# Performance work log

Hardware: AMD Instinct MI355X
Metric: run time of the kernel (lower is better)

## Reference

```python
import jax, jax.numpy as jnp
import numpy as np

B, D_IN, D_HID, E, K = 524288, 256, 512, 16, 2


def setup_inputs() -> dict:
    key = jax.random.key(0)
    kx, k1, kb1, k2, kb2 = jax.random.split(key, 5)
    s1 = 1.0 / np.sqrt(D_IN)
    s2 = 1.0 / np.sqrt(D_HID)
    return {
        "x": jax.random.normal(kx, (B, D_IN), dtype=jnp.float32),
        "w1": jax.random.uniform(k1, (D_IN, D_HID), jnp.float32, -s1, s1),
        "b1": jax.random.uniform(kb1, (D_HID,), jnp.float32, -s1, s1),
        "w2": jax.random.uniform(k2, (D_HID, E), jnp.float32, -s2, s2),
        "b2": jax.random.uniform(kb2, (E,), jnp.float32, -s2, s2),
    }


def reference(x, w1, b1, w2, b2):
    # 2-layer MLP router
    h = jax.nn.relu(x @ w1 + b1)            # [B, D_HID]
    logits = h @ w2 + b2                    # [B, E]
    # top-k mask (1.0 at top-k expert slots, 0.0 elsewhere)
    _, topk_idx = jax.lax.top_k(logits, K)  # [B, K]
    mask = jax.nn.one_hot(topk_idx, E, dtype=logits.dtype).sum(axis=-2)  # [B, E]
    # NOTE: faithful to original — non-topk logits are zeroed (not -inf),
    # then softmax is taken over ALL experts including the zeros.
    sparse_logits = logits * mask
    weights = jax.nn.softmax(sparse_logits, axis=-1)
    return weights
```

## Files before the change

### kernel.cpp

```cpp
#include <hip/hip_runtime.h>
#include <cmath>

#define NE   16
#define DIN  256
#define DHID 512
#define NROW 524288
#define TAU  4e-4f

typedef __bf16 bf16;
typedef bf16  bf16x8 __attribute__((ext_vector_type(8)));
typedef float f32x4  __attribute__((ext_vector_type(4)));

template<int CTRL>
__device__ __forceinline__ float dpp_xor_add(float v) {
    int s = __builtin_amdgcn_update_dpp(0, __float_as_int(v), CTRL, 0xF, 0xF, true);
    return v + __int_as_float(s);
}
template<int OFF>
__device__ __forceinline__ float swz_xor_add(float v) {
    int s = __builtin_amdgcn_ds_swizzle(__float_as_int(v), OFF);
    return v + __int_as_float(s);
}

__global__ __launch_bounds__(256)
void split_w1_k(const float* __restrict__ w1, bf16* __restrict__ t_hi,
                bf16* __restrict__ t_lo) {
    int i = blockIdx.x * 256 + threadIdx.x;
    int col = i & 511, k = i >> 9;
    float v = w1[k * DHID + col];
    bf16 h = (bf16)v;
    t_hi[col * DIN + k] = h;
    t_lo[col * DIN + k] = (bf16)(v - (float)h);
}

__global__ __launch_bounds__(256, 2)
void router_mfma_k(const float* __restrict__ x,
                   const float* __restrict__ b1,
                   const float* __restrict__ w2,
                   const float* __restrict__ b2,
                   float* __restrict__ out,
                   const bf16* __restrict__ w1t_hi,
                   const bf16* __restrict__ w1t_lo,
                   unsigned* __restrict__ cnt,
                   unsigned* __restrict__ ids,
                   unsigned cap)
{
    __shared__ __align__(16) bf16 xh_s[4][129][8];
    __shared__ __align__(16) bf16 xl_s[4][129][8];
    __shared__ __align__(16) bf16 wh_s[4][129][8];
    __shared__ __align__(16) bf16 wl_s[4][129][8];
    __shared__ float l_lds[128][NE + 1];

    const int t    = threadIdx.x;
    const int lane = t & 63;
    const int wv   = t >> 6;
    const int c    = lane & 15;
    const int g    = lane >> 4;
    const long long row0 = (long long)blockIdx.x * 128;

    float lg[8];
#pragma unroll
    for (int i = 0; i < 8; ++i) lg[i] = 0.f;

    for (int ch = 0; ch < 4; ++ch) {
        const int nh0 = ch * 128;
        f32x4 acc[2][8];
#pragma unroll
        for (int ti = 0; ti < 2; ++ti)
#pragma unroll
            for (int tj = 0; tj < 8; ++tj)
#pragma unroll
                for (int r = 0; r < 4; ++r) acc[ti][tj][r] = 0.f;

        for (int ks = 0; ks < 8; ++ks) {
            const int k0 = ks * 32;
            __syncthreads();
#pragma unroll
            for (int u = 0; u < 4; ++u) {
                int idx = u * 256 + t;
                int row = idx >> 3, f4 = idx & 7;
                float4 v = *(const float4*)(x + (row0 + row) * DIN + k0 + f4 * 4);
                int gg = f4 >> 1, j0 = (f4 & 1) * 4;
                bf16* dh = &xh_s[gg][row][j0];
                bf16* dl = &xl_s[gg][row][j0];
                float vv[4] = {v.x, v.y, v.z, v.w};
#pragma unroll
                for (int q = 0; q < 4; ++q) {
                    bf16 hb = (bf16)vv[q];
                    dh[q] = hb;
                    dl[q] = (bf16)(vv[q] - (float)hb);
                }
            }
            {
                int col = t >> 1, half = t & 1;
                const bf16* sh = w1t_hi + (nh0 + col) * DIN + k0 + 16 * half;
                const bf16* sl = w1t_lo + (nh0 + col) * DIN + k0 + 16 * half;
#pragma unroll
                for (int u = 0; u < 2; ++u) {
                    *(bf16x8*)&wh_s[2 * half + u][col][0] = *(const bf16x8*)(sh + 8 * u);
                    *(bf16x8*)&wl_s[2 * half + u][col][0] = *(const bf16x8*)(sl + 8 * u);
                }
            }
            __syncthreads();
            bf16x8 ah[2], al[2];
#pragma unroll
            for (int ti = 0; ti < 2; ++ti) {
                ah[ti] = *(const bf16x8*)&xh_s[g][32 * wv + 16 * ti + c][0];
                al[ti] = *(const bf16x8*)&xl_s[g][32 * wv + 16 * ti + c][0];
            }
#pragma unroll
            for (int tj = 0; tj < 8; ++tj) {
                bf16x8 bh = *(const bf16x8*)&wh_s[g][16 * tj + c][0];
                bf16x8 bl = *(const bf16x8*)&wl_s[g][16 * tj + c][0];
#pragma unroll
                for (int ti = 0; ti < 2; ++ti) {
                    acc[ti][tj] = __builtin_amdgcn_mfma_f32_16x16x32_bf16(ah[ti], bh, acc[ti][tj], 0, 0, 0);
                    acc[ti][tj] = __builtin_amdgcn_mfma_f32_16x16x32_bf16(ah[ti], bl, acc[ti][tj], 0, 0, 0);
                    acc[ti][tj] = __builtin_amdgcn_mfma_f32_16x16x32_bf16(al[ti], bh, acc[ti][tj], 0, 0, 0);
                }
            }
        }

#pragma unroll
        for (int tj = 0; tj < 8; ++tj) {
            float bj = b1[nh0 + 16 * tj + c];
#pragma unroll
            for (int ti = 0; ti < 2; ++ti)
#pragma unroll
                for (int r = 0; r < 4; ++r)
                    acc[ti][tj][r] = fmaxf(acc[ti][tj][r] + bj, 0.f);
        }

#pragma unroll 1
        for (int e = 0; e < NE; ++e) {
            float p[8];
#pragma unroll
            for (int i = 0; i < 8; ++i) p[i] = 0.f;
#pragma unroll
            for (int tj = 0; tj < 8; ++tj) {
                float wvv = w2[(nh0 + 16 * tj + c) * NE + e];
#pragma unroll
                for (int ti = 0; ti < 2; ++ti)
#pragma unroll
                    for (int r = 0; r < 4; ++r)
                        p[ti * 4 + r] = fmaf(acc[ti][tj][r], wvv, p[ti * 4 + r]);
            }
#pragma unroll
            for (int i = 0; i < 8; ++i) p[i] = dpp_xor_add<0xB1>(p[i]);
#pragma unroll
            for (int i = 0; i < 8; ++i) p[i] = dpp_xor_add<0x4E>(p[i]);
#pragma unroll
            for (int i = 0; i < 8; ++i) p[i] = swz_xor_add<0x101F>(p[i]);
#pragma unroll
            for (int i = 0; i < 8; ++i) p[i] = swz_xor_add<0x201F>(p[i]);
            if (c == e) {
#pragma unroll
                for (int i = 0; i < 8; ++i) lg[i] += p[i];
            }
        }
    }

    __syncthreads();
    {
        float b2c = b2[c];
#pragma unroll
        for (int ti = 0; ti < 2; ++ti)
#pragma unroll
            for (int r = 0; r < 4; ++r)
                l_lds[32 * wv + 16 * ti + 4 * g + r][c] = lg[ti * 4 + r] + b2c;
    }
    __syncthreads();

    if (t < 128) {
        float l[NE];
#pragma unroll
        for (int e = 0; e < NE; ++e) l[e] = l_lds[t][e];

        float m1 = -INFINITY; int i1 = 0;
#pragma unroll
        for (int e = 0; e < NE; ++e)
            if (l[e] > m1) { m1 = l[e]; i1 = e; }
        float m2 = -INFINITY; int i2 = -1;
#pragma unroll
        for (int e = 0; e < NE; ++e)
            if (e != i1 && l[e] > m2) { m2 = l[e]; i2 = e; }
        float m3 = -INFINITY;
#pragma unroll
        for (int e = 0; e < NE; ++e)
            if (e != i1 && e != i2 && l[e] > m3) m3 = l[e];

        if (m2 - m3 < TAU) {
            unsigned idx = atomicAdd(cnt, 1u);
            if (idx < cap) ids[idx] = (unsigned)(row0 + t);
        }

        float s[NE];
#pragma unroll
        for (int e = 0; e < NE; ++e)
            s[e] = (e == i1 || e == i2) ? l[e] : 0.f;
        float mx = s[0];
#pragma unroll
        for (int e = 1; e < NE; ++e) mx = fmaxf(mx, s[e]);
        float ex[NE];
        float sum = 0.f;
#pragma unroll
        for (int e = 0; e < NE; ++e) { ex[e] = expf(s[e] - mx); sum += ex[e]; }
        float* og = out + (row0 + t) * NE;
#pragma unroll
        for (int e = 0; e < NE; ++e) og[e] = ex[e] / sum;
    }
}

__global__ __launch_bounds__(256)
void fixup_k(const float* __restrict__ x,
             const float* __restrict__ w1,
             const float* __restrict__ b1,
             const float* __restrict__ w2,
             const float* __restrict__ b2,
             float* __restrict__ out,
             const unsigned* __restrict__ cntp,
             const unsigned* __restrict__ ids,
             unsigned cap)
{
    const int lane = threadIdx.x & 63;
    const int gw   = (int)((blockIdx.x * 256 + threadIdx.x) >> 6);
    const int nw   = (int)((gridDim.x * 256) >> 6);
    unsigned n = *cntp; if (n > cap) n = cap;
    const int c = lane & 15;
    const int g = lane >> 4;

    for (unsigned wi = gw; wi < n; wi += nw) {
        unsigned row = ids[wi];
        const float* xr = x + (size_t)row * DIN;
        const int nh0 = 128 * g;
        int cols[8];
#pragma unroll
        for (int j = 0; j < 8; ++j)
            cols[j] = nh0 + c * 4 + (j & 3) + ((j >> 2) << 6);

        float a[8];
#pragma unroll
        for (int j = 0; j < 8; ++j) a[j] = 0.f;
        for (int k4 = 0; k4 < 64; ++k4) {
            float4 xv = *(const float4*)(xr + k4 * 4);
            const float* wp = w1 + (size_t)(k4 * 4) * DHID;
#pragma unroll
            for (int j = 0; j < 8; ++j) {
                a[j] = fmaf(xv.x, wp[cols[j]],            a[j]);
                a[j] = fmaf(xv.y, wp[DHID + cols[j]],     a[j]);
                a[j] = fmaf(xv.z, wp[2 * DHID + cols[j]], a[j]);
                a[j] = fmaf(xv.w, wp[3 * DHID + cols[j]], a[j]);
            }
        }
        float h[8];
#pragma unroll
        for (int j = 0; j < 8; ++j) h[j] = fmaxf(a[j] + b1[cols[j]], 0.f);

        float l[NE];
#pragma unroll 1
        for (int e = 0; e < NE; ++e) {
            float p = 0.f;
#pragma unroll
            for (int j = 0; j < 8; ++j)
                p = fmaf(h[j], w2[cols[j] * NE + e], p);
            p += __shfl_xor(p, 1, 64);
            p += __shfl_xor(p, 2, 64);
            p += __shfl_xor(p, 4, 64);
            p += __shfl_xor(p, 8, 64);
            float t0 = __shfl(p, 0 * 16 + e, 64);
            float t1 = __shfl(p, 1 * 16 + e, 64);
            float t2 = __shfl(p, 2 * 16 + e, 64);
            float t3 = __shfl(p, 3 * 16 + e, 64);
            l[e] = (((t0 + t1) + t2) + t3) + b2[e];
        }

        if (lane == 0) {
            float m1 = -INFINITY; int i1 = 0;
#pragma unroll
            for (int e = 0; e < NE; ++e)
                if (l[e] > m1) { m1 = l[e]; i1 = e; }
            float m2 = -INFINITY; int i2 = -1;
#pragma unroll
            for (int e = 0; e < NE; ++e)
                if (e != i1 && l[e] > m2) { m2 = l[e]; i2 = e; }
            float s[NE];
#pragma unroll
            for (int e = 0; e < NE; ++e)
                s[e] = (e == i1 || e == i2) ? l[e] : 0.f;
            float mx = s[0];
#pragma unroll
            for (int e = 1; e < NE; ++e) mx = fmaxf(mx, s[e]);
            float ex[NE];
            float sum = 0.f;
#pragma unroll
            for (int e = 0; e < NE; ++e) { ex[e] = expf(s[e] - mx); sum += ex[e]; }
            float* og = out + (size_t)row * NE;
#pragma unroll
            for (int e = 0; e < NE; ++e) og[e] = ex[e] / sum;
        }
    }
}

extern "C" void kernel_launch(void* const* d_in, const int* in_sizes, int n_in,
                              void* d_out, int out_size, void* d_ws, size_t ws_size,
                              hipStream_t stream) {
    const float* x  = (const float*)d_in[0];
    const float* w1 = (const float*)d_in[1];
    const float* b1 = (const float*)d_in[2];
    const float* w2 = (const float*)d_in[3];
    const float* b2 = (const float*)d_in[4];
    float* outp = (float*)d_out;

    bf16*     w1t_hi = (bf16*)d_ws;
    bf16*     w1t_lo = (bf16*)((char*)d_ws + (256u << 10));
    unsigned* cnt    = (unsigned*)((char*)d_ws + (1u << 20));
    unsigned* ids    = (unsigned*)((char*)d_ws + (1u << 20) + 64);
    unsigned  cap    = 0;
    if (ws_size > (1u << 20) + 64)
        cap = (unsigned)((ws_size - (1u << 20) - 64) / 4);

    hipMemsetAsync((char*)d_ws + (1u << 20), 0, 4, stream);
    split_w1_k<<<dim3(512), dim3(256), 0, stream>>>(w1, w1t_hi, w1t_lo);
    router_mfma_k<<<dim3(NROW / 128), dim3(256), 0, stream>>>(
        x, b1, w2, b2, outp, w1t_hi, w1t_lo, cnt, ids, cap);
    fixup_k<<<dim3(256), dim3(256), 0, stream>>>(
        x, w1, b1, w2, b2, outp, cnt, ids, cap);
}
```

Baseline: 1.347 ms.

## Stage x once per block and stream pre-tiled W1 via direct LDS loads

Each block now handles 64 rows and converts its whole x tile to bf16 hi/lo once into shared memory, instead of re-reading and re-splitting x for every hidden chunk. W1 is pre-arranged into the exact LDS tile layout so it can be copied with global_load_lds, and waves are split 2x2 over rows and hidden columns, with partial logits summed through LDS. Output rows are written with vector stores. This cuts repeated global traffic on x at the cost of much larger shared memory per block and more W1 reloads per row.

```diff
diff --git a/kernel.cpp b/kernel.cpp
--- a/kernel.cpp
+++ b/kernel.cpp
@@ -5,6 +5,7 @@
 #define DIN  256
 #define DHID 512
 #define NROW 524288
+#define ROWS 64
 #define TAU  4e-4f
 
 typedef __bf16 bf16;
@@ -21,16 +22,24 @@
     int s = __builtin_amdgcn_ds_swizzle(__float_as_int(v), OFF);
     return v + __int_as_float(s);
 }
+__device__ __forceinline__ void load_lds16(const void* g, void* l) {
+    __builtin_amdgcn_global_load_lds(
+        (const __attribute__((address_space(1))) void*)g,
+        (__attribute__((address_space(3))) void*)l,
+        16, 0, 0);
+}
 
 __global__ __launch_bounds__(256)
-void split_w1_k(const float* __restrict__ w1, bf16* __restrict__ t_hi,
-                bf16* __restrict__ t_lo) {
+void split_w1_k(const float* __restrict__ w1, bf16* __restrict__ w1t) {
     int i = blockIdx.x * 256 + threadIdx.x;
     int col = i & 511, k = i >> 9;
     float v = w1[k * DHID + col];
     bf16 h = (bf16)v;
-    t_hi[col * DIN + k] = h;
-    t_lo[col * DIN + k] = (bf16)(v - (float)h);
+    bf16 l = (bf16)(v - (float)h);
+    int ch = col >> 7, cl = col & 127, ksk = k >> 5, g = (k >> 3) & 3, j = k & 7;
+    size_t base = (size_t)(ch * 8 + ksk) * 8192;
+    w1t[base +        g * 1024 + cl * 8 + j] = h;
+    w1t[base + 4096 + g * 1024 + cl * 8 + j] = l;
 }
 
 __global__ __launch_bounds__(256, 2)
@@ -39,79 +48,81 @@
                    const float* __restrict__ w2,
                    const float* __restrict__ b2,
                    float* __restrict__ out,
-                   const bf16* __restrict__ w1t_hi,
-                   const bf16* __restrict__ w1t_lo,
+                   const bf16* __restrict__ w1t,
                    unsigned* __restrict__ cnt,
                    unsigned* __restrict__ ids,
                    unsigned cap)
 {
-    __shared__ __align__(16) bf16 xh_s[4][129][8];
-    __shared__ __align__(16) bf16 xl_s[4][129][8];
-    __shared__ __align__(16) bf16 wh_s[4][129][8];
-    __shared__ __align__(16) bf16 wl_s[4][129][8];
-    __shared__ float l_lds[128][NE + 1];
+    __shared__ __align__(16) bf16 xh_s[8][4][ROWS][8];
+    __shared__ __align__(16) bf16 xl_s[8][4][ROWS][8];
+    __shared__ __align__(16) bf16 w_s[2][4][128][8];
+    float* l_lds = (float*)&w_s[0][0][0][0];
 
     const int t    = threadIdx.x;
     const int lane = t & 63;
     const int wv   = t >> 6;
+    const int wr   = wv >> 1;
+    const int wc   = wv & 1;
     const int c    = lane & 15;
     const int g    = lane >> 4;
-    const long long row0 = (long long)blockIdx.x * 128;
+    const long long row0 = (long long)blockIdx.x * ROWS;
+
+    {
+        const int r = t & 63;
+        const float* xg = x + (row0 + r) * DIN + wv * 64;
+#pragma unroll
+        for (int m = 0; m < 8; ++m) {
+            float4 v0 = ((const float4*)xg)[2 * m];
+            float4 v1 = ((const float4*)xg)[2 * m + 1];
+            int k   = wv * 64 + m * 8;
+            int ksk = k >> 5, gg = (k >> 3) & 3;
+            float vv[8] = {v0.x, v0.y, v0.z, v0.w, v1.x, v1.y, v1.z, v1.w};
+            bf16 hb[8], lb[8];
+#pragma unroll
+            for (int q = 0; q < 8; ++q) {
+                hb[q] = (bf16)vv[q];
+                lb[q] = (bf16)(vv[q] - (float)hb[q]);
+            }
+            *(bf16x8*)&xh_s[ksk][gg][r][0] = *(const bf16x8*)hb;
+            *(bf16x8*)&xl_s[ksk][gg][r][0] = *(const bf16x8*)lb;
+        }
+    }
 
     float lg[8];
 #pragma unroll
     for (int i = 0; i < 8; ++i) lg[i] = 0.f;
 
     for (int ch = 0; ch < 4; ++ch) {
-        const int nh0 = ch * 128;
-        f32x4 acc[2][8];
+        f32x4 acc[2][4];
 #pragma unroll
         for (int ti = 0; ti < 2; ++ti)
 #pragma unroll
-            for (int tj = 0; tj < 8; ++tj)
+            for (int tj = 0; tj < 4; ++tj)
 #pragma unroll
                 for (int r = 0; r < 4; ++r) acc[ti][tj][r] = 0.f;
 
-        for (int ks = 0; ks < 8; ++ks) {
-            const int k0 = ks * 32;
+        for (int ksk = 0; ksk < 8; ++ksk) {
             __syncthreads();
-#pragma unroll
-            for (int u = 0; u < 4; ++u) {
-                int idx = u * 256 + t;
-                int row = idx >> 3, f4 = idx & 7;
-                float4 v = *(const float4*)(x + (row0 + row) * DIN + k0 + f4 * 4);
-                int gg = f4 >> 1, j0 = (f4 & 1) * 4;
-                bf16* dh = &xh_s[gg][row][j0];
-                bf16* dl = &xl_s[gg][row][j0];
-                float vv[4] = {v.x, v.y, v.z, v.w};
-#pragma unroll
-                for (int q = 0; q < 4; ++q) {
-                    bf16 hb = (bf16)vv[q];
-                    dh[q] = hb;
-                    dl[q] = (bf16)(vv[q] - (float)hb);
-                }
-            }
             {
-                int col = t >> 1, half = t & 1;
-                const bf16* sh = w1t_hi + (nh0 + col) * DIN + k0 + 16 * half;
-                const bf16* sl = w1t_lo + (nh0 + col) * DIN + k0 + 16 * half;
-#pragma unroll
-                for (int u = 0; u < 2; ++u) {
-                    *(bf16x8*)&wh_s[2 * half + u][col][0] = *(const bf16x8*)(sh + 8 * u);
-                    *(bf16x8*)&wl_s[2 * half + u][col][0] = *(const bf16x8*)(sl + 8 * u);
-                }
+                const bf16* src = w1t + (size_t)(ch * 8 + ksk) * 8192
+                                      + wv * 2048 + lane * 8;
+                bf16* dst = ((bf16*)w_s) + wv * 2048;
+#pragma unroll
+                for (int p = 0; p < 4; ++p)
+                    load_lds16(src + p * 512, dst + p * 512);
             }
             __syncthreads();
+
             bf16x8 ah[2], al[2];
 #pragma unroll
             for (int ti = 0; ti < 2; ++ti) {
-                ah[ti] = *(const bf16x8*)&xh_s[g][32 * wv + 16 * ti + c][0];
-                al[ti] = *(const bf16x8*)&xl_s[g][32 * wv + 16 * ti + c][0];
-            }
-#pragma unroll
-            for (int tj = 0; tj < 8; ++tj) {
-                bf16x8 bh = *(const bf16x8*)&wh_s[g][16 * tj + c][0];
-                bf16x8 bl = *(const bf16x8*)&wl_s[g][16 * tj + c][0];
+                ah[ti] = *(const bf16x8*)&xh_s[ksk][g][32 * wr + 16 * ti + c][0];
+                al[ti] = *(const bf16x8*)&xl_s[ksk][g][32 * wr + 16 * ti + c][0];
+            }
+#pragma unroll
+            for (int tj = 0; tj < 4; ++tj) {
+                bf16x8 bh = *(const bf16x8*)&w_s[0][g][64 * wc + 16 * tj + c][0];
+                bf16x8 bl = *(const bf16x8*)&w_s[1][g][64 * wc + 16 * tj + c][0];
 #pragma unroll
                 for (int ti = 0; ti < 2; ++ti) {
                     acc[ti][tj] = __builtin_amdgcn_mfma_f32_16x16x32_bf16(ah[ti], bh, acc[ti][tj], 0, 0, 0);
@@ -122,8 +133,8 @@
         }
 
 #pragma unroll
-        for (int tj = 0; tj < 8; ++tj) {
-            float bj = b1[nh0 + 16 * tj + c];
+        for (int tj = 0; tj < 4; ++tj) {
+            float bj = b1[128 * ch + 64 * wc + 16 * tj + c];
 #pragma unroll
             for (int ti = 0; ti < 2; ++ti)
 #pragma unroll
@@ -137,8 +148,8 @@
 #pragma unroll
             for (int i = 0; i < 8; ++i) p[i] = 0.f;
 #pragma unroll
-            for (int tj = 0; tj < 8; ++tj) {
-                float wvv = w2[(nh0 + 16 * tj + c) * NE + e];
+            for (int tj = 0; tj < 4; ++tj) {
+                float wvv = w2[(128 * ch + 64 * wc + 16 * tj + c) * NE + e];
 #pragma unroll
                 for (int ti = 0; ti < 2; ++ti)
 #pragma unroll
@@ -161,20 +172,28 @@
     }
 
     __syncthreads();
-    {
+    if (wc == 0) {
         float b2c = b2[c];
 #pragma unroll
         for (int ti = 0; ti < 2; ++ti)
 #pragma unroll
             for (int r = 0; r < 4; ++r)
-                l_lds[32 * wv + 16 * ti + 4 * g + r][c] = lg[ti * 4 + r] + b2c;
+                l_lds[(32 * wr + 16 * ti + 4 * g + r) * (NE + 1) + c] = lg[ti * 4 + r] + b2c;
     }
     __syncthreads();
-
-    if (t < 128) {
+    if (wc == 1) {
+#pragma unroll
+        for (int ti = 0; ti < 2; ++ti)
+#pragma unroll
+            for (int r = 0; r < 4; ++r)
+                l_lds[(32 * wr + 16 * ti + 4 * g + r) * (NE + 1) + c] += lg[ti * 4 + r];
+    }
+    __syncthreads();
+
+    if (t < ROWS) {
         float l[NE];
 #pragma unroll
-        for (int e = 0; e < NE; ++e) l[e] = l_lds[t][e];
+        for (int e = 0; e < NE; ++e) l[e] = l_lds[t * (NE + 1) + e];
 
         float m1 = -INFINITY; int i1 = 0;
 #pragma unroll
@@ -205,9 +224,13 @@
         float sum = 0.f;
 #pragma unroll
         for (int e = 0; e < NE; ++e) { ex[e] = expf(s[e] - mx); sum += ex[e]; }
-        float* og = out + (row0 + t) * NE;
-#pragma unroll
-        for (int e = 0; e < NE; ++e) og[e] = ex[e] / sum;
+        float r = 1.f / sum;
+        float4 o0 = {ex[0] * r, ex[1] * r, ex[2] * r, ex[3] * r};
+        float4 o1 = {ex[4] * r, ex[5] * r, ex[6] * r, ex[7] * r};
+        float4 o2 = {ex[8] * r, ex[9] * r, ex[10] * r, ex[11] * r};
+        float4 o3 = {ex[12] * r, ex[13] * r, ex[14] * r, ex[15] * r};
+        float4* og = (float4*)(out + (row0 + t) * NE);
+        og[0] = o0; og[1] = o1; og[2] = o2; og[3] = o3;
     }
 }
 
@@ -311,18 +334,17 @@
     const float* b2 = (const float*)d_in[4];
     float* outp = (float*)d_out;
 
-    bf16*     w1t_hi = (bf16*)d_ws;
-    bf16*     w1t_lo = (bf16*)((char*)d_ws + (256u << 10));
-    unsigned* cnt    = (unsigned*)((char*)d_ws + (1u << 20));
-    unsigned* ids    = (unsigned*)((char*)d_ws + (1u << 20) + 64);
-    unsigned  cap    = 0;
+    bf16*     w1t = (bf16*)d_ws;
+    unsigned* cnt = (unsigned*)((char*)d_ws + (1u << 20));
+    unsigned* ids = (unsigned*)((char*)d_ws + (1u << 20) + 64);
+    unsigned  cap = 0;
     if (ws_size > (1u << 20) + 64)
         cap = (unsigned)((ws_size - (1u << 20) - 64) / 4);
 
     hipMemsetAsync((char*)d_ws + (1u << 20), 0, 4, stream);
-    split_w1_k<<<dim3(512), dim3(256), 0, stream>>>(w1, w1t_hi, w1t_lo);
-    router_mfma_k<<<dim3(NROW / 128), dim3(256), 0, stream>>>(
-        x, b1, w2, b2, outp, w1t_hi, w1t_lo, cnt, ids, cap);
+    split_w1_k<<<dim3(512), dim3(256), 0, stream>>>(w1, w1t);
+    router_mfma_k<<<dim3(NROW / ROWS), dim3(256), 0, stream>>>(
+        x, b1, w2, b2, outp, w1t, cnt, ids, cap);
     fixup_k<<<dim3(256), dim3(256), 0, stream>>>(
         x, w1, b1, w2, b2, outp, cnt, ids, cap);
 }
```

After: 1.399 ms. 3.9% more time.
